# Optimization experiments

Hardware: AMD Instinct MI355X
Metric: run time of the kernel (lower is better)

Reference implementation:

```python
import jax, jax.numpy as jnp
import numpy as np

MAX_REL = 8  # max_relative_position
B, H, L, D = 2, 16, 2048, 64


def setup_inputs() -> dict:
    key = jax.random.key(0)
    kq, kk, kv, kb = jax.random.split(key, 4)
    return {
        "q": jax.random.normal(kq, (B, H, L, D), dtype=jnp.float32),
        "k": jax.random.normal(kk, (B, H, L, D), dtype=jnp.float32),
        "v": jax.random.normal(kv, (B, H, L, D), dtype=jnp.float32),
        "relative_bias": jax.random.normal(kb, (2 * MAX_REL + 1,), dtype=jnp.float32),
    }


def reference(q, k, v, relative_bias):
    Bq, Hq, Lq, Dq = q.shape
    scale = jnp.sqrt(jnp.asarray(Dq, dtype=q.dtype))
    # [B,H,L,L] attention scores
    scores = jnp.einsum("bhqd,bhkd->bhqk", q, k) / scale
    pos = jnp.arange(Lq)
    rel = pos[None, :] - pos[:, None]                 # [L,L] (col - row), matches torch code
    idx = jnp.clip(rel, -MAX_REL, MAX_REL) + MAX_REL  # [L,L] in [0, 2*MAX_REL]
    bias = relative_bias[idx]                         # [L,L] gather from bias table
    scores = scores + bias[None, None, :, :]
    attn = jax.nn.softmax(scores, axis=-1)
    return jnp.einsum("bhqk,bhkd->bhqd", attn, v)
```

## Files before the change

### kernel.cpp

```cpp
#include <hip/hip_runtime.h>
#include <hip/hip_bf16.h>


#define LOG2E 1.44269504088896f

constexpr int Lv = 2048, Dv = 64;
constexpr int BH  = 32;
constexpr int BQ  = 128;
constexpr int BKT = 64;
constexpr int NQT = Lv / BQ;
constexpr int NKT = Lv / BKT;
constexpr int LDK = 72;
constexpr int LDO = 68;
constexpr int MAXREL = 8;

typedef __bf16 bf16x8 __attribute__((ext_vector_type(8)));
typedef __bf16 bf16x4 __attribute__((ext_vector_type(4)));
typedef float  f32x4  __attribute__((ext_vector_type(4)));

static __device__ __forceinline__ unsigned pack2bf(float a, float b) {
    __bf16 x = (__bf16)a, y = (__bf16)b;
    unsigned short ux = __builtin_bit_cast(unsigned short, x);
    unsigned short uy = __builtin_bit_cast(unsigned short, y);
    return (unsigned)ux | ((unsigned)uy << 16);
}

__global__
__attribute__((amdgpu_flat_work_group_size(512, 512), amdgpu_waves_per_eu(4, 4)))
void relattn_kernel(
    const float* __restrict__ Q, const float* __restrict__ K,
    const float* __restrict__ V, const float* __restrict__ RB,
    float* __restrict__ O)
{
    constexpr int SKBYTES  = 2 * BKT * LDK * 2;
    constexpr int SVBYTES  = 2 * Dv  * LDK * 2;
    constexpr int PADBYTES = 20480;
    __shared__ __align__(16) unsigned char smem[SKBYTES + SVBYTES + PADBYTES];
    __shared__ float sRB[2 * MAXREL + 1];
    __bf16* sK = (__bf16*)smem;
    __bf16* sV = (__bf16*)(smem + SKBYTES);

    const int tid  = threadIdx.x;
    const int w    = tid >> 6;
    const int lane = tid & 63;
    const int l16  = lane & 15;
    const int lg   = lane >> 4;
    const int pair = w >> 1;
    const int wh   = w & 1;

    const int bh = blockIdx.x & (BH - 1);
    const int qt = blockIdx.x >> 5;

    const size_t base = (size_t)bh * Lv * Dv;
    const float* Qb = Q + base + (size_t)qt * BQ * Dv;
    const float* Kb = K + base;
    const float* Vb = V + base;
    float*       Ob = O + base + (size_t)qt * BQ * Dv;

    if (tid < 2 * MAXREL + 1) sRB[tid] = RB[tid] * LOG2E;

    const float qsc = 0.125f * LOG2E;
    bf16x8 qfrag[2][2];
    #pragma unroll
    for (int h = 0; h < 2; ++h) {
        const float* qrow = Qb + (pair * 32 + h * 16 + l16) * Dv;
        #pragma unroll
        for (int s = 0; s < 2; ++s) {
            const float4 a = *(const float4*)(qrow + lg * 8 + 32 * s);
            const float4 b = *(const float4*)(qrow + lg * 8 + 32 * s + 4);
            bf16x8 f;
            f[0] = (__bf16)(a.x * qsc); f[1] = (__bf16)(a.y * qsc);
            f[2] = (__bf16)(a.z * qsc); f[3] = (__bf16)(a.w * qsc);
            f[4] = (__bf16)(b.x * qsc); f[5] = (__bf16)(b.y * qsc);
            f[6] = (__bf16)(b.z * qsc); f[7] = (__bf16)(b.w * qsc);
            qfrag[h][s] = f;
        }
    }

    f32x4 oacc[2][4];
    float lacc[2][2];
    #pragma unroll
    for (int h = 0; h < 2; ++h) {
        lacc[h][0] = 0.f; lacc[h][1] = 0.f;
        #pragma unroll
        for (int t = 0; t < 4; ++t)
            #pragma unroll
            for (int r = 0; r < 4; ++r) oacc[h][t][r] = 0.f;
    }

    const int kr0 = tid >> 4;
    const int kc4 = (tid & 15) * 4;
    const int vkk0 = (tid & 31) * 2;
    const int vd0  = (tid >> 5) * 4;
    const int vcol = (vkk0 & 35) | ((vkk0 & 12) << 1) | ((vkk0 & 16) >> 2);

    float4 kreg[2], vreg[2];

    auto loadKV = [&](int kt) {
        const float* Ks = Kb + (size_t)kt * BKT * Dv;
        const float* Vs = Vb + (size_t)kt * BKT * Dv;
        kreg[0] = *(const float4*)(Ks + kr0 * Dv + kc4);
        kreg[1] = *(const float4*)(Ks + (32 + kr0) * Dv + kc4);
        vreg[0] = *(const float4*)(Vs + vkk0 * Dv + vd0);
        vreg[1] = *(const float4*)(Vs + (vkk0 + 1) * Dv + vd0);
    };
    auto stageKV = [&](int buf) {
        __bf16* sKb = sK + buf * (BKT * LDK);
        __bf16* sVb = sV + buf * (Dv * LDK);
        #pragma unroll
        for (int p = 0; p < 2; ++p) {
            bf16x4 pk;
            pk[0] = (__bf16)kreg[p].x; pk[1] = (__bf16)kreg[p].y;
            pk[2] = (__bf16)kreg[p].z; pk[3] = (__bf16)kreg[p].w;
            *(bf16x4*)&sKb[(p * 32 + kr0) * LDK + kc4] = pk;
        }
        #pragma unroll
        for (int j = 0; j < 4; ++j)
            *(unsigned*)&sVb[(vd0 + j) * LDK + vcol] =
                pack2bf(vreg[0][j], vreg[1][j]);
    };

    loadKV(0);
    stageKV(0);
    __syncthreads();

    const int qw0 = qt * BQ + pair * 32;
    const int qgl = qw0 + l16;

    for (int kt = 0; kt < NKT; ++kt) {
        const int buf = kt & 1;
        __bf16* sKb = sK + buf * (BKT * LDK);
        __bf16* sVb = sV + buf * (Dv * LDK);

        if (kt + 1 < NKT) loadKV(kt + 1);

        f32x4 sacc[2][2];
        #pragma unroll
        for (int h = 0; h < 2; ++h)
            #pragma unroll
            for (int tl = 0; tl < 2; ++tl)
                #pragma unroll
                for (int r = 0; r < 4; ++r) sacc[h][tl][r] = 0.f;
        __builtin_amdgcn_s_setprio(1);
        #pragma unroll
        for (int s = 0; s < 2; ++s) {
            #pragma unroll
            for (int tl = 0; tl < 2; ++tl) {
                bf16x8 a = *(const bf16x8*)&sKb[((2 * wh + tl) * 16 + l16) * LDK + lg * 8 + 32 * s];
                sacc[0][tl] = __builtin_amdgcn_mfma_f32_16x16x32_bf16(a, qfrag[0][s], sacc[0][tl], 0, 0, 0);
                sacc[1][tl] = __builtin_amdgcn_mfma_f32_16x16x32_bf16(a, qfrag[1][s], sacc[1][tl], 0, 0, 0);
            }
        }
        __builtin_amdgcn_s_setprio(0);

        if (kt + 1 < NKT) stageKV(buf ^ 1);

        const int k0 = kt * BKT + wh * 32;
        bf16x8 pfrag[2];
        #pragma unroll
        for (int h = 0; h < 2; ++h) {
            const int qlo = qw0 + h * 16;
            if (k0 >= qlo + 15 + MAXREL) {
                const float bc = sRB[2 * MAXREL];
                #pragma unroll
                for (int tl = 0; tl < 2; ++tl)
                    #pragma unroll
                    for (int r = 0; r < 4; ++r) {
                        float p = __builtin_amdgcn_exp2f(sacc[h][tl][r] + bc);
                        lacc[h][r & 1] += p;
                        pfrag[h][tl * 4 + r] = (__bf16)p;
                    }
            } else if (k0 + 31 + MAXREL <= qlo) {
                const float bc = sRB[0];
                #pragma unroll
                for (int tl = 0; tl < 2; ++tl)
                    #pragma unroll
                    for (int r = 0; r < 4; ++r) {
                        float p = __builtin_amdgcn_exp2f(sacc[h][tl][r] + bc);
                        lacc[h][r & 1] += p;
                        pfrag[h][tl * 4 + r] = (__bf16)p;
                    }
            } else {
                const int kkb = k0 + lg * 4 - (qgl + h * 16);
                #pragma unroll
                for (int tl = 0; tl < 2; ++tl) {
                    #pragma unroll
                    for (int r = 0; r < 4; ++r) {
                        int d = kkb + tl * 16 + r;
                        d = d < -MAXREL ? -MAXREL : (d > MAXREL ? MAXREL : d);
                        float p = __builtin_amdgcn_exp2f(sacc[h][tl][r] + sRB[d + MAXREL]);
                        lacc[h][r & 1] += p;
                        pfrag[h][tl * 4 + r] = (__bf16)p;
                    }
                }
            }
        }

        __builtin_amdgcn_s_setprio(1);
        #pragma unroll
        for (int t = 0; t < 4; ++t) {
            bf16x8 vf = *(const bf16x8*)&sVb[(t * 16 + l16) * LDK + lg * 8 + 32 * wh];
            oacc[0][t] = __builtin_amdgcn_mfma_f32_16x16x32_bf16(vf, pfrag[0], oacc[0][t], 0, 0, 0);
            oacc[1][t] = __builtin_amdgcn_mfma_f32_16x16x32_bf16(vf, pfrag[1], oacc[1][t], 0, 0, 0);
        }
        __builtin_amdgcn_s_setprio(0);

        __syncthreads();
    }

    float lh[2];
    #pragma unroll
    for (int h = 0; h < 2; ++h) {
        float l = lacc[h][0] + lacc[h][1];
        l += __shfl_xor(l, 16);
        l += __shfl_xor(l, 32);
        lh[h] = l;
    }

    __syncthreads();
    float* sO = (float*)smem;
    float* sL = (float*)(smem + 4 * 32 * LDO * 4);
    if (wh == 1) {
        #pragma unroll
        for (int h = 0; h < 2; ++h) {
            #pragma unroll
            for (int t = 0; t < 4; ++t)
                *(f32x4*)&sO[(pair * 32 + h * 16 + l16) * LDO + t * 16 + lg * 4] = oacc[h][t];
            if (lg == 0) sL[pair * 32 + h * 16 + l16] = lh[h];
        }
    }
    __syncthreads();
    if (wh == 0) {
        #pragma unroll
        for (int h = 0; h < 2; ++h) {
            const float lt = lh[h] + sL[pair * 32 + h * 16 + l16];
            const float linv = 1.f / lt;
            float* orow = Ob + (pair * 32 + h * 16 + l16) * Dv;
            #pragma unroll
            for (int t = 0; t < 4; ++t) {
                f32x4 oo = *(const f32x4*)&sO[(pair * 32 + h * 16 + l16) * LDO + t * 16 + lg * 4];
                float4 o;
                o.x = (oacc[h][t][0] + oo[0]) * linv;
                o.y = (oacc[h][t][1] + oo[1]) * linv;
                o.z = (oacc[h][t][2] + oo[2]) * linv;
                o.w = (oacc[h][t][3] + oo[3]) * linv;
                *(float4*)(orow + t * 16 + lg * 4) = o;
            }
        }
    }
}

extern "C" void kernel_launch(void* const* d_in, const int* in_sizes, int n_in,
                              void* d_out, int out_size, void* d_ws, size_t ws_size,
                              hipStream_t stream) {
    const float* q  = (const float*)d_in[0];
    const float* k  = (const float*)d_in[1];
    const float* v  = (const float*)d_in[2];
    const float* rb = (const float*)d_in[3];
    float* out = (float*)d_out;
    relattn_kernel<<<dim3(BH * NQT), dim3(512), 0, stream>>>(q, k, v, rb, out);
}
```

Measured before the change: 141.8 us.

## Software-pipeline QK of next tile against softmax and PV of previous tile

Restructures the K-loop so the QK MFMAs for tile kt run alongside the softmax and PV of tile kt-1, using two score register sets that alternate roles. V gets a triple-buffered LDS ring and K stays double-buffered, with global loads issued two tiles ahead. The setprio hints are removed and the LDS padding is cut to offset the extra V buffer. The goal is to hide exp and LDS latency behind matrix work, at the cost of more live registers under a fixed waves-per-EU target, which could cause spills.

After: 206.0 us. 45.2% more time.

```diff
diff --git a/kernel.cpp b/kernel.cpp
--- a/kernel.cpp
+++ b/kernel.cpp
@@ -32,13 +32,13 @@
     const float* __restrict__ V, const float* __restrict__ RB,
     float* __restrict__ O)
 {
-    constexpr int SKBYTES  = 2 * BKT * LDK * 2;
-    constexpr int SVBYTES  = 2 * Dv  * LDK * 2;
-    constexpr int PADBYTES = 20480;
-    __shared__ __align__(16) unsigned char smem[SKBYTES + SVBYTES + PADBYTES];
+    constexpr int KBYTES   = 2 * BKT * LDK * 2;
+    constexpr int VBYTES   = 3 * Dv  * LDK * 2;
+    constexpr int PADBYTES = 10240;
+    __shared__ __align__(16) unsigned char smem[KBYTES + VBYTES + PADBYTES];
     __shared__ float sRB[2 * MAXREL + 1];
     __bf16* sK = (__bf16*)smem;
-    __bf16* sV = (__bf16*)(smem + SKBYTES);
+    __bf16* sV = (__bf16*)(smem + KBYTES);
 
     const int tid  = threadIdx.x;
     const int w    = tid >> 6;
@@ -104,9 +104,9 @@
         vreg[0] = *(const float4*)(Vs + vkk0 * Dv + vd0);
         vreg[1] = *(const float4*)(Vs + (vkk0 + 1) * Dv + vd0);
     };
-    auto stageKV = [&](int buf) {
-        __bf16* sKb = sK + buf * (BKT * LDK);
-        __bf16* sVb = sV + buf * (Dv * LDK);
+    auto stageKV = [&](int kb, int vslot) {
+        __bf16* sKb = sK + kb * (BKT * LDK);
+        __bf16* sVb = sV + vslot * (Dv * LDK);
         #pragma unroll
         for (int p = 0; p < 2; ++p) {
             bf16x4 pk;
@@ -120,43 +120,11 @@
                 pack2bf(vreg[0][j], vreg[1][j]);
     };
 
-    loadKV(0);
-    stageKV(0);
-    __syncthreads();
-
     const int qw0 = qt * BQ + pair * 32;
     const int qgl = qw0 + l16;
 
-    for (int kt = 0; kt < NKT; ++kt) {
-        const int buf = kt & 1;
-        __bf16* sKb = sK + buf * (BKT * LDK);
-        __bf16* sVb = sV + buf * (Dv * LDK);
-
-        if (kt + 1 < NKT) loadKV(kt + 1);
-
-        f32x4 sacc[2][2];
-        #pragma unroll
-        for (int h = 0; h < 2; ++h)
-            #pragma unroll
-            for (int tl = 0; tl < 2; ++tl)
-                #pragma unroll
-                for (int r = 0; r < 4; ++r) sacc[h][tl][r] = 0.f;
-        __builtin_amdgcn_s_setprio(1);
-        #pragma unroll
-        for (int s = 0; s < 2; ++s) {
-            #pragma unroll
-            for (int tl = 0; tl < 2; ++tl) {
-                bf16x8 a = *(const bf16x8*)&sKb[((2 * wh + tl) * 16 + l16) * LDK + lg * 8 + 32 * s];
-                sacc[0][tl] = __builtin_amdgcn_mfma_f32_16x16x32_bf16(a, qfrag[0][s], sacc[0][tl], 0, 0, 0);
-                sacc[1][tl] = __builtin_amdgcn_mfma_f32_16x16x32_bf16(a, qfrag[1][s], sacc[1][tl], 0, 0, 0);
-            }
-        }
-        __builtin_amdgcn_s_setprio(0);
-
-        if (kt + 1 < NKT) stageKV(buf ^ 1);
-
-        const int k0 = kt * BKT + wh * 32;
-        bf16x8 pfrag[2];
+    auto softmax = [&](int ktp, f32x4 (&sacc)[2][2], bf16x8 (&pfrag)[2]) {
+        const int k0 = ktp * BKT + wh * 32;
         #pragma unroll
         for (int h = 0; h < 2; ++h) {
             const int qlo = qw0 + h * 16;
@@ -195,17 +163,72 @@
                 }
             }
         }
-
-        __builtin_amdgcn_s_setprio(1);
+    };
+
+    auto qk = [&](int kt, f32x4 (&cur)[2][2]) {
+        __bf16* sKb = sK + (kt & 1) * (BKT * LDK);
+        #pragma unroll
+        for (int h = 0; h < 2; ++h)
+            #pragma unroll
+            for (int tl = 0; tl < 2; ++tl)
+                #pragma unroll
+                for (int r = 0; r < 4; ++r) cur[h][tl][r] = 0.f;
+        #pragma unroll
+        for (int s = 0; s < 2; ++s) {
+            #pragma unroll
+            for (int tl = 0; tl < 2; ++tl) {
+                bf16x8 a = *(const bf16x8*)&sKb[((2 * wh + tl) * 16 + l16) * LDK + lg * 8 + 32 * s];
+                cur[0][tl] = __builtin_amdgcn_mfma_f32_16x16x32_bf16(a, qfrag[0][s], cur[0][tl], 0, 0, 0);
+                cur[1][tl] = __builtin_amdgcn_mfma_f32_16x16x32_bf16(a, qfrag[1][s], cur[1][tl], 0, 0, 0);
+            }
+        }
+    };
+
+    auto pv = [&](int vslot, bf16x8 (&pfrag)[2]) {
+        __bf16* sVr = sV + vslot * (Dv * LDK);
         #pragma unroll
         for (int t = 0; t < 4; ++t) {
-            bf16x8 vf = *(const bf16x8*)&sVb[(t * 16 + l16) * LDK + lg * 8 + 32 * wh];
+            bf16x8 vf = *(const bf16x8*)&sVr[(t * 16 + l16) * LDK + lg * 8 + 32 * wh];
             oacc[0][t] = __builtin_amdgcn_mfma_f32_16x16x32_bf16(vf, pfrag[0], oacc[0][t], 0, 0, 0);
             oacc[1][t] = __builtin_amdgcn_mfma_f32_16x16x32_bf16(vf, pfrag[1], oacc[1][t], 0, 0, 0);
         }
-        __builtin_amdgcn_s_setprio(0);
-
+    };
+
+    f32x4 sA[2][2], sB[2][2];
+
+    loadKV(0);
+    stageKV(0, 0);
+    loadKV(1);
+    __syncthreads();
+    qk(0, sA);
+    stageKV(1, 1);
+    loadKV(2);
+    __syncthreads();
+
+    auto ITER = [&](int kt, f32x4 (&cur)[2][2], f32x4 (&prev)[2][2],
+                    int rs, int ws) {
+        qk(kt, cur);
+        bf16x8 pfrag[2];
+        softmax(kt - 1, prev, pfrag);
+        if (kt + 1 < NKT) stageKV((kt + 1) & 1, ws);
+        if (kt + 2 < NKT) loadKV(kt + 2);
+        pv(rs, pfrag);
         __syncthreads();
+    };
+
+    int rs = 0, ws = 2;
+    for (int k2 = 1; k2 < NKT - 1; k2 += 2) {
+        ITER(k2,     sB, sA, rs, ws);
+        rs = (rs == 2) ? 0 : rs + 1; ws = (ws == 2) ? 0 : ws + 1;
+        ITER(k2 + 1, sA, sB, rs, ws);
+        rs = (rs == 2) ? 0 : rs + 1; ws = (ws == 2) ? 0 : ws + 1;
+    }
+    ITER(NKT - 1, sB, sA, rs, ws);
+
+    {
+        bf16x8 pfrag[2];
+        softmax(NKT - 1, sB, pfrag);
+        pv((NKT - 1) % 3, pfrag);
     }
 
     float lh[2];
```
